# Performance work log

Hardware: AMD Instinct MI355X
Metric: run time of the kernel (lower is better)

The kernel has to match this reference:

```python
import jax, jax.numpy as jnp
import numpy as np

B, T = 256, 20          # batch, sequence length
D = 128                 # encoder feature dim
H = 256                 # LSTM controller hidden / controller_output_size
KS = 256                # memory key/word size
MEM = 20                # memory slots
KNN = 4                 # k-NN addressing
Y = 4                   # output classes (y_dim)
EPS = 1e-8


def setup_inputs() -> dict:
    key = jax.random.key(0)
    ks = jax.random.split(key, 16)
    def kn(k, shape, fan_in):  # kaiming-normal-ish init
        return jax.random.normal(k, shape, jnp.float32) * np.float32(np.sqrt(2.0 / fan_in))
    return {
        "x": jax.random.normal(ks[0], (B, T, 32, 32), jnp.float32),
        # conv encoder
        "conv1_w": kn(ks[1], (32, 1, 4, 4), 1 * 16),  "conv1_b": jnp.zeros(32, jnp.float32),
        "conv2_w": kn(ks[2], (32, 32, 4, 4), 32 * 16), "conv2_b": jnp.zeros(32, jnp.float32),
        "conv3_w": kn(ks[3], (32, 32, 4, 4), 32 * 16), "conv3_b": jnp.zeros(32, jnp.float32),
        "fc1_w": kn(ks[4], (256, 512), 512), "fc1_b": jnp.zeros(256, jnp.float32),
        "fc2_w": kn(ks[5], (128, 256), 256), "fc2_b": jnp.zeros(128, jnp.float32),
        # context norm
        "gamma": jnp.ones(D, jnp.float32), "beta": jnp.zeros(D, jnp.float32),
        # LSTM controller: input = [z_t(128), read(256)] = 384
        "lstm_wi": kn(ks[6], (4 * H, D + KS), D + KS),
        "lstm_wh": kn(ks[7], (4 * H, H), H),
        "lstm_b": jnp.zeros(4 * H, jnp.float32),
        # head projections
        "wk": kn(ks[8], (KS, H), H),   # read key
        "wwk": kn(ks[9], (KS, H), H),  # write key
        "wv": kn(ks[10], (KS, H), H),  # write value
        # output layer on [h, read]
        "wo": kn(ks[11], (Y, H + KS), H + KS), "wo_b": jnp.zeros(Y, jnp.float32),
        "mem_init": jax.random.normal(ks[12], (MEM, KS), jnp.float32) * 0.01,
    }


def _conv(h, w, b):
    out = jax.lax.conv_general_dilated(h, w, (2, 2), [(1, 1), (1, 1)],
                                       dimension_numbers=("NCHW", "OIHW", "NCHW"))
    return jax.nn.relu(out + b[None, :, None, None])


def reference(x, conv1_w, conv1_b, conv2_w, conv2_b, conv3_w, conv3_b,
              fc1_w, fc1_b, fc2_w, fc2_b, gamma, beta,
              lstm_wi, lstm_wh, lstm_b, wk, wwk, wv, wo, wo_b, mem_init):
    b, t = x.shape[0], x.shape[1]
    # --- conv encoder on all B*T frames ---
    h = x.reshape(-1, 1, 32, 32)
    h = _conv(h, conv1_w, conv1_b)          # [BT,32,16,16]
    h = _conv(h, conv2_w, conv2_b)          # [BT,32,8,8]
    h = _conv(h, conv3_w, conv3_b)          # [BT,32,4,4]
    h = h.reshape(h.shape[0], -1)           # [BT,512] (NCHW flatten, matches torch)
    h = jax.nn.relu(h @ fc1_w.T + fc1_b)
    z = jax.nn.relu(h @ fc2_w.T + fc2_b).reshape(b, t, D)
    # --- context norm over time dim (torch var is unbiased) ---
    mu = z.mean(1)
    sigma = jnp.sqrt(z.var(1, ddof=1) + EPS)
    z = (z - mu[:, None, :]) / sigma[:, None, :] * gamma + beta
    # --- NTM-style MANN with k-NN addressing, scan over time ---
    zt = jnp.swapaxes(z, 0, 1)              # [T,B,D]
    M0 = jnp.broadcast_to(mem_init, (b, MEM, KS)) + jnp.zeros((b, MEM, KS), jnp.float32)
    carry0 = (jnp.zeros((b, H), jnp.float32), jnp.zeros((b, H), jnp.float32),
              jnp.zeros((b, KS), jnp.float32), M0)

    def step(carry, z_t):
        h_, c_, r_, M = carry
        inp = jnp.concatenate([z_t, r_], -1)
        gates = inp @ lstm_wi.T + h_ @ lstm_wh.T + lstm_b
        ig, fg, gg, og = jnp.split(gates, 4, -1)  # torch LSTM gate order i,f,g,o
        c_ = jax.nn.sigmoid(fg) * c_ + jax.nn.sigmoid(ig) * jnp.tanh(gg)
        h_ = jax.nn.sigmoid(og) * jnp.tanh(c_)
        Mn = M / (jnp.linalg.norm(M, axis=-1, keepdims=True) + EPS)
        def knn(kq):  # cosine sim -> top-k -> softmax weights
            kqn = kq / (jnp.linalg.norm(kq, axis=-1, keepdims=True) + EPS)
            sims = jnp.einsum('bd,bnd->bn', kqn, Mn)
            tv, ti = jax.lax.top_k(sims, KNN)
            return jax.nn.softmax(tv, -1), ti
        # read head
        wr, ir = knn(h_ @ wk.T)
        rows = jnp.take_along_axis(M, ir[..., None], axis=1)   # [B,KNN,KS] gather
        r_new = jnp.einsum('bk,bkd->bd', wr, rows)
        # write head: weighted scatter-add into top-k slots
        ws, iw = knn(h_ @ wwk.T)
        v = jnp.tanh(h_ @ wv.T)
        bidx = jnp.arange(M.shape[0])[:, None]
        M = M.at[bidx, iw].add(ws[..., None] * v[:, None, :])
        y = jnp.concatenate([h_, r_new], -1) @ wo.T + wo_b
        return (h_, c_, r_new, M), y

    _, ys = jax.lax.scan(step, carry0, zt)   # ys: [T,B,Y]
    y_pred_linear = ys[-1]
    return y_pred_linear, jnp.argmax(y_pred_linear, 1)
```

## Files before the change

### kernel.cpp

```cpp
#include <hip/hip_runtime.h>
#include <hip/hip_bf16.h>

#define EPSF 1e-8f

#define OFF_WIT 0
#define N_WIT   393216
#define OFF_WHT 393216
#define N_WHT   262144
#define OFF_PKT 655360
#define N_PKT   196608
#define OFF_F1T 851968
#define N_F1T   131072
#define OFF_F2T 983040
#define N_F2T   32768
#define OFF_Z   1015808
#define N_Z     655360
#define WS_BASE 1671168
#define OFF_GZ  1671168
#define N_GZ    5242880
#define WS_FULL 6914048

__global__ __launch_bounds__(256) void pack_kernel(
    const float* __restrict__ wi, const float* __restrict__ wh,
    const float* __restrict__ wk, const float* __restrict__ wwk,
    const float* __restrict__ wv,
    const float* __restrict__ f1w, const float* __restrict__ f2w,
    float* __restrict__ ws) {
  int id = blockIdx.x * 256 + threadIdx.x;
  if (id < N_WIT) {
    int j = id & 3, r = (id >> 2) & 1023, k4 = id >> 12;
    ws[OFF_WIT + id] = wi[r * 384 + k4 * 4 + j];
    return;
  }
  id -= N_WIT;
  if (id < N_WHT) {
    int j = id & 3, r = (id >> 2) & 1023, k4 = id >> 12;
    ws[OFF_WHT + id] = wh[r * 256 + k4 * 4 + j];
    return;
  }
  id -= N_WHT;
  if (id < N_PKT) {
    int j = id & 3;
    int q = id >> 2;
    int c = q % 768, k4 = q / 768;
    int m = c >> 8, o = c & 255;
    int col = o * 256 + k4 * 4 + j;
    float v = (m == 0) ? wk[col] : (m == 1) ? wwk[col] : wv[col];
    ws[OFF_PKT + id] = v;
    return;
  }
  id -= N_PKT;
  if (id < N_F1T) {
    int m = id & 3, o = (id >> 2) & 255, k4 = id >> 10;
    ws[OFF_F1T + id] = f1w[o * 512 + k4 * 4 + m];
    return;
  }
  id -= N_F1T;
  if (id < N_F2T) {
    int m = id & 3, o = (id >> 2) & 127, k4 = id >> 9;
    ws[OFF_F2T + id] = f2w[o * 256 + k4 * 4 + m];
  }
}

__global__ __launch_bounds__(256) void enc_kernel(
    const float* __restrict__ x,
    const float* __restrict__ w1, const float* __restrict__ b1,
    const float* __restrict__ w2, const float* __restrict__ b2,
    const float* __restrict__ w3, const float* __restrict__ b3,
    const float* __restrict__ f1b, const float* __restrict__ f2b,
    float* __restrict__ ws) {
  __shared__ __align__(16) float xs[1024];
  __shared__ __align__(16) float c1s[512 * 19];
  __shared__ __align__(16) float c2s[256 * 9];
  __shared__ __align__(16) float c3s[512];
  __shared__ __align__(16) float h1s[256];

  const float4* __restrict__ f1T4 = (const float4*)(ws + OFF_F1T);
  const float4* __restrict__ f2T4 = (const float4*)(ws + OFF_F2T);
  float* __restrict__ z = ws + OFF_Z;

  const int f = blockIdx.x;
  const int tid = threadIdx.x;

  for (int i = tid; i < 1024; i += 256) xs[i] = x[f * 1024 + i];
  __syncthreads();

  {
    int oy = tid >> 4, ox = tid & 15;
    float patch[16];
    #pragma unroll
    for (int ky = 0; ky < 4; ++ky) {
      int iy = oy * 2 - 1 + ky;
      #pragma unroll
      for (int kx = 0; kx < 4; ++kx) {
        int ix = ox * 2 - 1 + kx;
        patch[ky * 4 + kx] =
            ((unsigned)iy <= 31u && (unsigned)ix <= 31u) ? xs[iy * 32 + ix] : 0.f;
      }
    }
    for (int oc = 0; oc < 32; ++oc) {
      float acc = b1[oc];
      #pragma unroll
      for (int k = 0; k < 16; ++k) acc = fmaf(patch[k], w1[oc * 16 + k], acc);
      c1s[(oc * 16 + oy) * 19 + ox] = fmaxf(acc, 0.f);
    }
  }
  __syncthreads();

  {
    int pix = tid & 63;
    int og = __builtin_amdgcn_readfirstlane(tid >> 6);
    int oy = pix >> 3, ox = pix & 7;
    float acc[8];
    #pragma unroll
    for (int j = 0; j < 8; ++j) acc[j] = b2[og * 8 + j];
    for (int ic = 0; ic < 32; ++ic) {
      float patch[16];
      #pragma unroll
      for (int ky = 0; ky < 4; ++ky) {
        int iy = oy * 2 - 1 + ky;
        #pragma unroll
        for (int kx = 0; kx < 4; ++kx) {
          int ix = ox * 2 - 1 + kx;
          patch[ky * 4 + kx] = ((unsigned)iy <= 15u && (unsigned)ix <= 15u)
                                   ? c1s[(ic * 16 + iy) * 19 + ix] : 0.f;
        }
      }
      #pragma unroll
      for (int j = 0; j < 8; ++j) {
        const float* wr = w2 + ((og * 8 + j) * 32 + ic) * 16;
        #pragma unroll
        for (int k = 0; k < 16; ++k) acc[j] = fmaf(patch[k], wr[k], acc[j]);
      }
    }
    #pragma unroll
    for (int j = 0; j < 8; ++j)
      c2s[((og * 8 + j) * 8 + oy) * 9 + ox] = fmaxf(acc[j], 0.f);
  }
  __syncthreads();

  {
    int pix = tid & 15, grp = tid >> 4;
    int oy = pix >> 2, ox = pix & 3;
    float a0 = b3[grp * 2], a1 = b3[grp * 2 + 1];
    for (int ic = 0; ic < 32; ++ic) {
      float patch[16];
      #pragma unroll
      for (int ky = 0; ky < 4; ++ky) {
        int iy = oy * 2 - 1 + ky;
        #pragma unroll
        for (int kx = 0; kx < 4; ++kx) {
          int ix = ox * 2 - 1 + kx;
          patch[ky * 4 + kx] = ((unsigned)iy <= 7u && (unsigned)ix <= 7u)
                                   ? c2s[(ic * 8 + iy) * 9 + ix] : 0.f;
        }
      }
      const float4* wa = (const float4*)(w3 + ((grp * 2 + 0) * 32 + ic) * 16);
      const float4* wb = (const float4*)(w3 + ((grp * 2 + 1) * 32 + ic) * 16);
      #pragma unroll
      for (int q = 0; q < 4; ++q) {
        float4 qa = wa[q], qb = wb[q];
        a0 = fmaf(patch[q * 4 + 0], qa.x, a0);
        a0 = fmaf(patch[q * 4 + 1], qa.y, a0);
        a0 = fmaf(patch[q * 4 + 2], qa.z, a0);
        a0 = fmaf(patch[q * 4 + 3], qa.w, a0);
        a1 = fmaf(patch[q * 4 + 0], qb.x, a1);
        a1 = fmaf(patch[q * 4 + 1], qb.y, a1);
        a1 = fmaf(patch[q * 4 + 2], qb.z, a1);
        a1 = fmaf(patch[q * 4 + 3], qb.w, a1);
      }
    }
    c3s[(grp * 2 + 0) * 16 + pix] = fmaxf(a0, 0.f);
    c3s[(grp * 2 + 1) * 16 + pix] = fmaxf(a1, 0.f);
  }
  __syncthreads();

  {
    float acc = f1b[tid];
    #pragma unroll 8
    for (int k4 = 0; k4 < 128; ++k4) {
      float4 cv = ((const float4*)c3s)[k4];
      float4 w = f1T4[k4 * 256 + tid];
      acc = fmaf(w.x, cv.x, acc);
      acc = fmaf(w.y, cv.y, acc);
      acc = fmaf(w.z, cv.z, acc);
      acc = fmaf(w.w, cv.w, acc);
    }
    h1s[tid] = fmaxf(acc, 0.f);
  }
  __syncthreads();

  if (tid < 128) {
    float acc = f2b[tid];
    #pragma unroll 8
    for (int k4 = 0; k4 < 64; ++k4) {
      float4 hv = ((const float4*)h1s)[k4];
      float4 w = f2T4[k4 * 128 + tid];
      acc = fmaf(w.x, hv.x, acc);
      acc = fmaf(w.y, hv.y, acc);
      acc = fmaf(w.z, hv.z, acc);
      acc = fmaf(w.w, hv.w, acc);
    }
    z[f * 128 + tid] = fmaxf(acc, 0.f);
  }
}

__global__ __launch_bounds__(256) void norm_kernel(
    float* __restrict__ ws,
    const float* __restrict__ gamma, const float* __restrict__ beta) {
  float* z = ws + OFF_Z;
  int g = blockIdx.x * 256 + threadIdx.x;
  int b = g >> 7, d = g & 127;
  float vals[20];
  float mu = 0.f;
  #pragma unroll
  for (int t = 0; t < 20; ++t) {
    float v = z[(b * 20 + t) * 128 + d];
    vals[t] = v;
    mu += v;
  }
  mu *= (1.f / 20.f);
  float var = 0.f;
  #pragma unroll
  for (int t = 0; t < 20; ++t) {
    float dd = vals[t] - mu;
    var = fmaf(dd, dd, var);
  }
  var *= (1.f / 19.f);
  float inv = 1.f / sqrtf(var + EPSF);
  float ga = gamma[d], be = beta[d];
  #pragma unroll
  for (int t = 0; t < 20; ++t)
    z[(b * 20 + t) * 128 + d] = fmaf((vals[t] - mu) * inv, ga, be);
}

__global__ __launch_bounds__(512) void gz_kernel(
    const float* __restrict__ ws, const float* __restrict__ lb,
    float* __restrict__ gz) {
  __shared__ __align__(16) float zs[16][128];
  const float4* wiT4 = (const float4*)(ws + OFF_WIT);
  const float* zz = ws + OFF_Z;
  const int tid = threadIdx.x;
  const int f0 = blockIdx.x * 16;

  for (int i = tid; i < 2048; i += 512) zs[i >> 7][i & 127] = zz[f0 * 128 + i];
  __syncthreads();

  float acc0[16], acc1[16];
  const float b0v = lb[tid], b1v = lb[tid + 512];
  #pragma unroll
  for (int f = 0; f < 16; ++f) { acc0[f] = b0v; acc1[f] = b1v; }

  for (int k4 = 0; k4 < 32; ++k4) {
    float4 w0 = wiT4[k4 * 1024 + tid];
    float4 w1 = wiT4[k4 * 1024 + tid + 512];
    #pragma unroll
    for (int f = 0; f < 16; ++f) {
      float4 zv = *(const float4*)&zs[f][k4 * 4];
      acc0[f] = fmaf(w0.x, zv.x, acc0[f]);
      acc0[f] = fmaf(w0.y, zv.y, acc0[f]);
      acc0[f] = fmaf(w0.z, zv.z, acc0[f]);
      acc0[f] = fmaf(w0.w, zv.w, acc0[f]);
      acc1[f] = fmaf(w1.x, zv.x, acc1[f]);
      acc1[f] = fmaf(w1.y, zv.y, acc1[f]);
      acc1[f] = fmaf(w1.z, zv.z, acc1[f]);
      acc1[f] = fmaf(w1.w, zv.w, acc1[f]);
    }
  }
  #pragma unroll
  for (int f = 0; f < 16; ++f) {
    gz[(f0 + f) * 1024 + tid] = acc0[f];
    gz[(f0 + f) * 1024 + 512 + tid] = acc1[f];
  }
}

__global__ __launch_bounds__(1024, 2) void scan_kernel(
    const float* __restrict__ ws, const float* __restrict__ gz,
    const float* __restrict__ lb, const float* __restrict__ wo,
    const float* __restrict__ wob, const float* __restrict__ mem_init,
    float* __restrict__ out) {
  __shared__ float Msh[2][20 * 257];
  __shared__ __align__(16) float gsh[2][1024];
  __shared__ __align__(16) float inp[2][384];
  __shared__ __align__(16) float hsh[2][256];
  __shared__ float kqsh[2][2][256];
  __shared__ float vsh[2][256];
  __shared__ float sims[2][2][20];
  __shared__ float invq[2][2];
  __shared__ float wsel[2][2][4];
  __shared__ int isel[2][2][4];
  __shared__ float ysh[2][4];

  const int r = threadIdx.x;
  const int b0 = blockIdx.x * 2;
  const int rot = ((blockIdx.x >> 3) & 15) << 2;
  const float4* wiT4 = (const float4*)(ws + OFF_WIT);
  const float4* whT4 = (const float4*)(ws + OFF_WHT);
  const float4* pkT4 = (const float4*)(ws + OFF_PKT);
  const float* zz = ws + OFF_Z;
  const int k4s = gz ? 32 : 0;
  const int wiRange = 96 - k4s;

  #pragma unroll
  for (int bl = 0; bl < 2; ++bl)
    for (int idx = r; idx < 5120; idx += 1024)
      Msh[bl][(idx >> 8) * 257 + (idx & 255)] = mem_init[idx];
  if (r < 512) {
    int bl = r >> 8, u = r & 255;
    hsh[bl][u] = 0.f;
    inp[bl][128 + u] = 0.f;
  }
  float c_reg = 0.f;
  const float bias = lb[r];
  __syncthreads();

  for (int t = 0; t < 20; ++t) {
    if (!gz && r < 256) {
      int bl = r >> 7, d = r & 127;
      inp[bl][d] = zz[((b0 + bl) * 20 + t) * 128 + d];
    }
    __syncthreads();

    float a0, a1;
    if (gz) {
      a0 = gz[(b0 * 20 + t) * 1024 + r];
      a1 = gz[((b0 + 1) * 20 + t) * 1024 + r];
    } else {
      a0 = bias;
      a1 = bias;
    }
    {
      const float4* ip0 = (const float4*)inp[0];
      const float4* ip1 = (const float4*)inp[1];
      #pragma unroll 8
      for (int j = 0; j < 64; ++j) {
        int kk = j + rot;
        if (kk >= 64) kk -= 64;
        int k4 = k4s + kk;
        if (k4s == 0 && j == 0) {  }
        float4 w = wiT4[k4 * 1024 + r];
        float4 z0 = ip0[k4], z1 = ip1[k4];
        a0 = fmaf(w.x, z0.x, a0); a1 = fmaf(w.x, z1.x, a1);
        a0 = fmaf(w.y, z0.y, a0); a1 = fmaf(w.y, z1.y, a1);
        a0 = fmaf(w.z, z0.z, a0); a1 = fmaf(w.z, z1.z, a1);
        a0 = fmaf(w.w, z0.w, a0); a1 = fmaf(w.w, z1.w, a1);
      }
      if (!gz) {
        #pragma unroll 8
        for (int k4 = 0; k4 < 32; ++k4) {
          float4 w = wiT4[k4 * 1024 + r];
          float4 z0 = ip0[k4], z1 = ip1[k4];
          a0 = fmaf(w.x, z0.x, a0); a1 = fmaf(w.x, z1.x, a1);
          a0 = fmaf(w.y, z0.y, a0); a1 = fmaf(w.y, z1.y, a1);
          a0 = fmaf(w.z, z0.z, a0); a1 = fmaf(w.z, z1.z, a1);
          a0 = fmaf(w.w, z0.w, a0); a1 = fmaf(w.w, z1.w, a1);
        }
      }
      const float4* hp0 = (const float4*)hsh[0];
      const float4* hp1 = (const float4*)hsh[1];
      #pragma unroll 8
      for (int j = 0; j < 64; ++j) {
        int k4 = j + rot;
        if (k4 >= 64) k4 -= 64;
        float4 w = whT4[k4 * 1024 + r];
        float4 h0 = hp0[k4], h1 = hp1[k4];
        a0 = fmaf(w.x, h0.x, a0); a1 = fmaf(w.x, h1.x, a1);
        a0 = fmaf(w.y, h0.y, a0); a1 = fmaf(w.y, h1.y, a1);
        a0 = fmaf(w.z, h0.z, a0); a1 = fmaf(w.z, h1.z, a1);
        a0 = fmaf(w.w, h0.w, a0); a1 = fmaf(w.w, h1.w, a1);
      }
    }
    gsh[0][r] = a0;
    gsh[1][r] = a1;
    __syncthreads();

    if (r < 512) {
      int bl = r >> 8, u = r & 255;
      float ig = gsh[bl][u], fg = gsh[bl][256 + u];
      float gg = gsh[bl][512 + u], og = gsh[bl][768 + u];
      c_reg = (1.f / (1.f + expf(-fg))) * c_reg +
              (1.f / (1.f + expf(-ig))) * tanhf(gg);
      hsh[bl][u] = (1.f / (1.f + expf(-og))) * tanhf(c_reg);
    }
    __syncthreads();

    if (r < 768) {
      int m = r >> 8, o = r & 255;
      float s0 = 0.f, s1 = 0.f;
      const float4* hp0 = (const float4*)hsh[0];
      const float4* hp1 = (const float4*)hsh[1];
      #pragma unroll 8
      for (int j = 0; j < 64; ++j) {
        int k4 = j + rot;
        if (k4 >= 64) k4 -= 64;
        float4 w = pkT4[k4 * 768 + r];
        float4 h0 = hp0[k4], h1 = hp1[k4];
        s0 = fmaf(w.x, h0.x, s0); s1 = fmaf(w.x, h1.x, s1);
        s0 = fmaf(w.y, h0.y, s0); s1 = fmaf(w.y, h1.y, s1);
        s0 = fmaf(w.z, h0.z, s0); s1 = fmaf(w.z, h1.z, s1);
        s0 = fmaf(w.w, h0.w, s0); s1 = fmaf(w.w, h1.w, s1);
      }
      if (m < 2) {
        kqsh[0][m][o] = s0;
        kqsh[1][m][o] = s1;
      } else {
        vsh[0][o] = tanhf(s0);
        vsh[1][o] = tanhf(s1);
      }
    }
    __syncthreads();

    if (r < 320) {
      int bl = r >= 160;
      int q = bl ? r - 160 : r;
      int n = q >> 3, l = q & 7;
      const float* Mr = &Msh[bl][n * 257];
      float ss = 0.f, s1 = 0.f, s2 = 0.f;
      for (int i = 0; i < 32; ++i) {
        int k = l + 8 * i;
        float m = Mr[k];
        ss = fmaf(m, m, ss);
        s1 = fmaf(kqsh[bl][0][k], m, s1);
        s2 = fmaf(kqsh[bl][1][k], m, s2);
      }
      ss += __shfl_xor(ss, 1); s1 += __shfl_xor(s1, 1); s2 += __shfl_xor(s2, 1);
      ss += __shfl_xor(ss, 2); s1 += __shfl_xor(s1, 2); s2 += __shfl_xor(s2, 2);
      ss += __shfl_xor(ss, 4); s1 += __shfl_xor(s1, 4); s2 += __shfl_xor(s2, 4);
      if (l == 0) {
        float inv = 1.f / (sqrtf(ss) + EPSF);
        sims[bl][0][n] = s1 * inv;
        sims[bl][1][n] = s2 * inv;
      }
    } else if (r < 324) {
      int bl2 = (r - 320) >> 1, hd = r & 1;
      float qq = 0.f;
      for (int k = 0; k < 256; ++k) {
        float q = kqsh[bl2][hd][k];
        qq = fmaf(q, q, qq);
      }
      invq[bl2][hd] = 1.f / (sqrtf(qq) + EPSF);
    }
    __syncthreads();

    if (r < 4) {
      int bl = r >> 1, hd = r & 1;
      const float* sm = sims[bl][hd];
      float inv = invq[bl][hd];
      unsigned mask = 0;
      float tv[4];
      int ti[4];
      for (int j = 0; j < 4; ++j) {
        float best = -3.4e38f;
        int bx = 0;
        for (int n = 0; n < 20; ++n)
          if (!((mask >> n) & 1u) && sm[n] > best) { best = sm[n]; bx = n; }
        mask |= 1u << bx;
        tv[j] = best * inv;
        ti[j] = bx;
      }
      float e0 = 1.f;
      float e1 = expf(tv[1] - tv[0]);
      float e2 = expf(tv[2] - tv[0]);
      float e3 = expf(tv[3] - tv[0]);
      float s = e0 + e1 + e2 + e3;
      wsel[bl][hd][0] = e0 / s; wsel[bl][hd][1] = e1 / s;
      wsel[bl][hd][2] = e2 / s; wsel[bl][hd][3] = e3 / s;
      isel[bl][hd][0] = ti[0]; isel[bl][hd][1] = ti[1];
      isel[bl][hd][2] = ti[2]; isel[bl][hd][3] = ti[3];
    }
    __syncthreads();

    if (r < 512) {
      int bl = r >> 8, u = r & 255;
      float rvv = 0.f;
      #pragma unroll
      for (int j = 0; j < 4; ++j)
        rvv = fmaf(wsel[bl][0][j], Msh[bl][isel[bl][0][j] * 257 + u], rvv);
      float vv = vsh[bl][u];
      #pragma unroll
      for (int j = 0; j < 4; ++j)
        Msh[bl][isel[bl][1][j] * 257 + u] += wsel[bl][1][j] * vv;
      inp[bl][128 + u] = rvv;
    }
    __syncthreads();
  }

  if (r < 8) {
    int bl = r >> 2, o = r & 3;
    float acc = wob[o];
    const float* wr = wo + o * 512;
    for (int k = 0; k < 256; ++k) acc = fmaf(wr[k], hsh[bl][k], acc);
    for (int k = 0; k < 256; ++k) acc = fmaf(wr[256 + k], inp[bl][128 + k], acc);
    ysh[bl][o] = acc;
    out[(b0 + bl) * 4 + o] = acc;
  }
  __syncthreads();
  if (r < 2) {
    float best = ysh[r][0];
    int bx = 0;
    #pragma unroll
    for (int o = 1; o < 4; ++o)
      if (ysh[r][o] > best) { best = ysh[r][o]; bx = o; }
    out[1024 + b0 + r] = (float)bx;
  }
}

__global__ __launch_bounds__(256) void fused_kernel(
    const float* __restrict__ x,
    const float* __restrict__ w1, const float* __restrict__ b1,
    const float* __restrict__ w2, const float* __restrict__ b2,
    const float* __restrict__ w3, const float* __restrict__ b3,
    const float* __restrict__ f1w, const float* __restrict__ f1b,
    const float* __restrict__ f2w, const float* __restrict__ f2b,
    const float* __restrict__ gamma, const float* __restrict__ beta,
    const float* __restrict__ wi, const float* __restrict__ wh,
    const float* __restrict__ lb, const float* __restrict__ wk,
    const float* __restrict__ wwk, const float* __restrict__ wv,
    const float* __restrict__ wo, const float* __restrict__ wob,
    const float* __restrict__ mem_init, float* __restrict__ out) {
  __shared__ float smem[15104];
  __shared__ float simr[20], simw[20], invq[2], wsel[2][4], ysh[4];
  __shared__ int isel[2][4];
  float* z_all = smem;
  float* pool = smem + 2560;
  float* xs = pool;
  float* c1s = pool + 1024;
  float* c2s = pool + 9216;
  float* c3s = pool + 11264;
  float* h1s = pool + 11776;
  float* w1s = pool + 12032;
  float* Msh = pool;
  float* inp = pool + 5140;
  float* hsh = pool + 5524;
  float* kqr = pool + 5780;
  float* kqw = pool + 6036;
  float* vsh = pool + 6292;
  const int tid = threadIdx.x;
  const int b = blockIdx.x;
  for (int i = tid; i < 512; i += 256) w1s[i] = w1[i];
  for (int f = 0; f < 20; ++f) {
    for (int i = tid; i < 1024; i += 256) xs[i] = x[(b * 20 + f) * 1024 + i];
    __syncthreads();
    for (int i = 0; i < 32; ++i) {
      int idx = i * 256 + tid;
      int oc = idx >> 8, pix = idx & 255, oy = pix >> 4, ox = pix & 15;
      float acc = b1[oc];
      for (int ky = 0; ky < 4; ++ky) {
        int iy = oy * 2 - 1 + ky;
        if ((unsigned)iy > 31u) continue;
        for (int kx = 0; kx < 4; ++kx) {
          int ix = ox * 2 - 1 + kx;
          if ((unsigned)ix > 31u) continue;
          acc = fmaf(xs[iy * 32 + ix], w1s[oc * 16 + ky * 4 + kx], acc);
        }
      }
      c1s[idx] = fmaxf(acc, 0.f);
    }
    __syncthreads();
    {
      int oc = tid >> 3, pg = tid & 7;
      float acc[8];
      float bb = b2[oc];
      for (int i = 0; i < 8; ++i) acc[i] = bb;
      for (int ic = 0; ic < 32; ++ic) {
        const float* in = &c1s[ic * 256];
        const float* wv_ = &w2[(oc * 32 + ic) * 16];
        for (int i = 0; i < 8; ++i) {
          int p = pg + 8 * i;
          int oy = p >> 3, ox = p & 7;
          for (int ky = 0; ky < 4; ++ky) {
            int iy = oy * 2 - 1 + ky;
            if ((unsigned)iy > 15u) continue;
            for (int kx = 0; kx < 4; ++kx) {
              int ix = ox * 2 - 1 + kx;
              if ((unsigned)ix > 15u) continue;
              acc[i] = fmaf(in[iy * 16 + ix], wv_[ky * 4 + kx], acc[i]);
            }
          }
        }
      }
      for (int i = 0; i < 8; ++i) c2s[oc * 64 + pg + 8 * i] = fmaxf(acc[i], 0.f);
    }
    __syncthreads();
    {
      int oc = tid >> 3, pg = tid & 7;
      float bb = b3[oc];
      float acc0 = bb, acc1 = bb;
      int p0 = pg, p1 = pg + 8;
      int oy0 = p0 >> 2, ox0 = p0 & 3, oy1 = p1 >> 2, ox1 = p1 & 3;
      for (int ic = 0; ic < 32; ++ic) {
        const float* in = &c2s[ic * 64];
        const float* wv_ = &w3[(oc * 32 + ic) * 16];
        for (int ky = 0; ky < 4; ++ky) {
          int iy0 = oy0 * 2 - 1 + ky, iy1 = oy1 * 2 - 1 + ky;
          for (int kx = 0; kx < 4; ++kx) {
            float w = wv_[ky * 4 + kx];
            int ix0 = ox0 * 2 - 1 + kx, ix1 = ox1 * 2 - 1 + kx;
            if ((unsigned)iy0 <= 7u && (unsigned)ix0 <= 7u)
              acc0 = fmaf(in[iy0 * 8 + ix0], w, acc0);
            if ((unsigned)iy1 <= 7u && (unsigned)ix1 <= 7u)
              acc1 = fmaf(in[iy1 * 8 + ix1], w, acc1);
          }
        }
      }
      c3s[oc * 16 + p0] = fmaxf(acc0, 0.f);
      c3s[oc * 16 + p1] = fmaxf(acc1, 0.f);
    }
    __syncthreads();
    {
      float acc = f1b[tid];
      const float* wr = f1w + tid * 512;
      for (int k = 0; k < 512; ++k) acc = fmaf(wr[k], c3s[k], acc);
      h1s[tid] = fmaxf(acc, 0.f);
    }
    __syncthreads();
    if (tid < 128) {
      float acc = f2b[tid];
      const float* wr = f2w + tid * 256;
      for (int k = 0; k < 256; ++k) acc = fmaf(wr[k], h1s[k], acc);
      z_all[f * 128 + tid] = fmaxf(acc, 0.f);
    }
    __syncthreads();
  }
  if (tid < 128) {
    float mu = 0.f;
    for (int t = 0; t < 20; ++t) mu += z_all[t * 128 + tid];
    mu *= (1.f / 20.f);
    float var = 0.f;
    for (int t = 0; t < 20; ++t) {
      float dd = z_all[t * 128 + tid] - mu;
      var = fmaf(dd, dd, var);
    }
    var *= (1.f / 19.f);
    float inv = 1.f / sqrtf(var + EPSF);
    float ga = gamma[tid], be = beta[tid];
    for (int t = 0; t < 20; ++t)
      z_all[t * 128 + tid] = fmaf((z_all[t * 128 + tid] - mu) * inv, ga, be);
  }
  for (int idx = tid; idx < 20 * 256; idx += 256)
    Msh[(idx >> 8) * 257 + (idx & 255)] = mem_init[idx];
  hsh[tid] = 0.f;
  inp[128 + tid] = 0.f;
  float c_reg = 0.f;
  __syncthreads();
  const int u = tid;
  for (int t = 0; t < 20; ++t) {
    if (u < 128) inp[u] = z_all[t * 128 + u];
    __syncthreads();
    float a[4];
    for (int g = 0; g < 4; ++g) {
      int row = g * 256 + u;
      float acc = lb[row];
      const float* wr = wi + row * 384;
      for (int k = 0; k < 384; ++k) acc = fmaf(wr[k], inp[k], acc);
      const float* hr = wh + row * 256;
      for (int k = 0; k < 256; ++k) acc = fmaf(hr[k], hsh[k], acc);
      a[g] = acc;
    }
    __syncthreads();
    {
      float ig = 1.f / (1.f + expf(-a[0]));
      float fg = 1.f / (1.f + expf(-a[1]));
      float gg = tanhf(a[2]);
      float og = 1.f / (1.f + expf(-a[3]));
      c_reg = fg * c_reg + ig * gg;
      hsh[u] = og * tanhf(c_reg);
    }
    __syncthreads();
    {
      float sk = 0.f, sw = 0.f, sv = 0.f;
      const float* rk = wk + u * 256;
      const float* rw = wwk + u * 256;
      const float* rv = wv + u * 256;
      for (int k = 0; k < 256; ++k) {
        float hv = hsh[k];
        sk = fmaf(rk[k], hv, sk);
        sw = fmaf(rw[k], hv, sw);
        sv = fmaf(rv[k], hv, sv);
      }
      kqr[u] = sk;
      kqw[u] = sw;
      vsh[u] = tanhf(sv);
    }
    __syncthreads();
    if (u < 20) {
      const float* Mr = &Msh[u * 257];
      float ss = 0.f, s1 = 0.f, s2 = 0.f;
      for (int k = 0; k < 256; ++k) {
        float m = Mr[k];
        ss = fmaf(m, m, ss);
        s1 = fmaf(kqr[k], m, s1);
        s2 = fmaf(kqw[k], m, s2);
      }
      float inv = 1.f / (sqrtf(ss) + EPSF);
      simr[u] = s1 * inv;
      simw[u] = s2 * inv;
    } else if (u == 20 || u == 21) {
      const float* q = (u == 20) ? kqr : kqw;
      float qq = 0.f;
      for (int k = 0; k < 256; ++k) qq = fmaf(q[k], q[k], qq);
      invq[u - 20] = 1.f / (sqrtf(qq) + EPSF);
    }
    __syncthreads();
    if (u < 2) {
      const float* sims = (u == 0) ? simr : simw;
      float inv = invq[u];
      unsigned mask = 0;
      float tv[4];
      int ti[4];
      for (int j = 0; j < 4; ++j) {
        float best = -3.4e38f;
        int bx = 0;
        for (int n = 0; n < 20; ++n)
          if (!((mask >> n) & 1u) && sims[n] > best) { best = sims[n]; bx = n; }
        mask |= 1u << bx;
        tv[j] = best * inv;
        ti[j] = bx;
      }
      float e1 = expf(tv[1] - tv[0]);
      float e2 = expf(tv[2] - tv[0]);
      float e3 = expf(tv[3] - tv[0]);
      float s = 1.f + e1 + e2 + e3;
      wsel[u][0] = 1.f / s; wsel[u][1] = e1 / s; wsel[u][2] = e2 / s; wsel[u][3] = e3 / s;
      isel[u][0] = ti[0]; isel[u][1] = ti[1]; isel[u][2] = ti[2]; isel[u][3] = ti[3];
    }
    __syncthreads();
    {
      float rvv = 0.f;
      for (int j = 0; j < 4; ++j)
        rvv = fmaf(wsel[0][j], Msh[isel[0][j] * 257 + u], rvv);
      float vv = vsh[u];
      for (int j = 0; j < 4; ++j)
        Msh[isel[1][j] * 257 + u] += wsel[1][j] * vv;
      inp[128 + u] = rvv;
    }
    __syncthreads();
  }
  if (u < 4) {
    float acc = wob[u];
    const float* wr = wo + u * 512;
    for (int k = 0; k < 256; ++k) acc = fmaf(wr[k], hsh[k], acc);
    for (int k = 0; k < 256; ++k) acc = fmaf(wr[256 + k], inp[128 + k], acc);
    ysh[u] = acc;
    out[b * 4 + u] = acc;
  }
  __syncthreads();
  if (u == 0) {
    float best = ysh[0];
    int bx = 0;
    for (int o = 1; o < 4; ++o)
      if (ysh[o] > best) { best = ysh[o]; bx = o; }
    out[1024 + b] = (float)bx;
  }
}

extern "C" void kernel_launch(void* const* d_in, const int* in_sizes, int n_in,
                              void* d_out, int out_size, void* d_ws, size_t ws_size,
                              hipStream_t stream) {
  const float* x    = (const float*)d_in[0];
  const float* c1w  = (const float*)d_in[1];
  const float* c1b  = (const float*)d_in[2];
  const float* c2w  = (const float*)d_in[3];
  const float* c2b  = (const float*)d_in[4];
  const float* c3w  = (const float*)d_in[5];
  const float* c3b  = (const float*)d_in[6];
  const float* f1w  = (const float*)d_in[7];
  const float* f1b  = (const float*)d_in[8];
  const float* f2w  = (const float*)d_in[9];
  const float* f2b  = (const float*)d_in[10];
  const float* gam  = (const float*)d_in[11];
  const float* bet  = (const float*)d_in[12];
  const float* wi   = (const float*)d_in[13];
  const float* wh   = (const float*)d_in[14];
  const float* lb   = (const float*)d_in[15];
  const float* wk   = (const float*)d_in[16];
  const float* wwk  = (const float*)d_in[17];
  const float* wv   = (const float*)d_in[18];
  const float* wo   = (const float*)d_in[19];
  const float* wob  = (const float*)d_in[20];
  const float* mem0 = (const float*)d_in[21];
  float* out = (float*)d_out;

  if (ws_size >= (size_t)WS_BASE * sizeof(float)) {
    float* ws = (float*)d_ws;
    const bool full = ws_size >= (size_t)WS_FULL * sizeof(float);
    pack_kernel<<<3968, 256, 0, stream>>>(wi, wh, wk, wwk, wv, f1w, f2w, ws);
    enc_kernel<<<5120, 256, 0, stream>>>(x, c1w, c1b, c2w, c2b, c3w, c3b,
                                         f1b, f2b, ws);
    norm_kernel<<<128, 256, 0, stream>>>(ws, gam, bet);
    const float* gz = nullptr;
    if (full) {
      gz_kernel<<<320, 512, 0, stream>>>(ws, lb, ws + OFF_GZ);
      gz = ws + OFF_GZ;
    }
    scan_kernel<<<128, 1024, 0, stream>>>(ws, gz, lb, wo, wob, mem0, out);
  } else {
    fused_kernel<<<256, 256, 0, stream>>>(x, c1w, c1b, c2w, c2b, c3w, c3b,
                                          f1w, f1b, f2w, f2b, gam, bet,
                                          wi, wh, lb, wk, wwk, wv, wo, wob,
                                          mem0, out);
  }
}
```

Before: 1.277 ms.

## Batch four frames per encoder block for FC weight reuse; nontemporal scan weight loads

The encoder kernel now runs the conv stack for four frames in sequence inside each block and keeps their conv3 and fc1 outputs in shared memory. The fc1 and fc2 layers then load each weight float4 once and apply it to all four frames, cutting global weight traffic for those layers by four. The grid shrinks from 5120 to 1280 blocks, which lowers parallelism for the conv part. Separately, the scan kernel's LSTM and projection weight loads use nontemporal load builtins, which changes their cache behaviour.

```diff
diff --git a/kernel.cpp b/kernel.cpp
--- a/kernel.cpp
+++ b/kernel.cpp
@@ -2,6 +2,8 @@
 #include <hip/hip_bf16.h>
 
 #define EPSF 1e-8f
+
+typedef float nt4 __attribute__((ext_vector_type(4)));
 
 #define OFF_WIT 0
 #define N_WIT   393216
@@ -72,49 +74,22 @@
   __shared__ __align__(16) float xs[1024];
   __shared__ __align__(16) float c1s[512 * 19];
   __shared__ __align__(16) float c2s[256 * 9];
-  __shared__ __align__(16) float c3s[512];
-  __shared__ __align__(16) float h1s[256];
+  __shared__ __align__(16) float c3s[4][512];
+  __shared__ __align__(16) float h1s[4][256];
 
   const float4* __restrict__ f1T4 = (const float4*)(ws + OFF_F1T);
   const float4* __restrict__ f2T4 = (const float4*)(ws + OFF_F2T);
   float* __restrict__ z = ws + OFF_Z;
 
-  const int f = blockIdx.x;
   const int tid = threadIdx.x;
 
-  for (int i = tid; i < 1024; i += 256) xs[i] = x[f * 1024 + i];
-  __syncthreads();
-
-  {
-    int oy = tid >> 4, ox = tid & 15;
-    float patch[16];
-    #pragma unroll
-    for (int ky = 0; ky < 4; ++ky) {
-      int iy = oy * 2 - 1 + ky;
-      #pragma unroll
-      for (int kx = 0; kx < 4; ++kx) {
-        int ix = ox * 2 - 1 + kx;
-        patch[ky * 4 + kx] =
-            ((unsigned)iy <= 31u && (unsigned)ix <= 31u) ? xs[iy * 32 + ix] : 0.f;
-      }
-    }
-    for (int oc = 0; oc < 32; ++oc) {
-      float acc = b1[oc];
-      #pragma unroll
-      for (int k = 0; k < 16; ++k) acc = fmaf(patch[k], w1[oc * 16 + k], acc);
-      c1s[(oc * 16 + oy) * 19 + ox] = fmaxf(acc, 0.f);
-    }
-  }
-  __syncthreads();
-
-  {
-    int pix = tid & 63;
-    int og = __builtin_amdgcn_readfirstlane(tid >> 6);
-    int oy = pix >> 3, ox = pix & 7;
-    float acc[8];
-    #pragma unroll
-    for (int j = 0; j < 8; ++j) acc[j] = b2[og * 8 + j];
-    for (int ic = 0; ic < 32; ++ic) {
+  for (int ff = 0; ff < 4; ++ff) {
+    const int f = blockIdx.x * 4 + ff;
+    for (int i = tid; i < 1024; i += 256) xs[i] = x[f * 1024 + i];
+    __syncthreads();
+
+    {
+      int oy = tid >> 4, ox = tid & 15;
       float patch[16];
       #pragma unroll
       for (int ky = 0; ky < 4; ++ky) {
@@ -122,86 +97,130 @@
         #pragma unroll
         for (int kx = 0; kx < 4; ++kx) {
           int ix = ox * 2 - 1 + kx;
-          patch[ky * 4 + kx] = ((unsigned)iy <= 15u && (unsigned)ix <= 15u)
-                                   ? c1s[(ic * 16 + iy) * 19 + ix] : 0.f;
+          patch[ky * 4 + kx] =
+              ((unsigned)iy <= 31u && (unsigned)ix <= 31u) ? xs[iy * 32 + ix] : 0.f;
         }
       }
+      for (int oc = 0; oc < 32; ++oc) {
+        float acc = b1[oc];
+        #pragma unroll
+        for (int k = 0; k < 16; ++k) acc = fmaf(patch[k], w1[oc * 16 + k], acc);
+        c1s[(oc * 16 + oy) * 19 + ox] = fmaxf(acc, 0.f);
+      }
+    }
+    __syncthreads();
+
+    {
+      int pix = tid & 63;
+      int og = __builtin_amdgcn_readfirstlane(tid >> 6);
+      int oy = pix >> 3, ox = pix & 7;
+      float acc[8];
       #pragma unroll
-      for (int j = 0; j < 8; ++j) {
-        const float* wr = w2 + ((og * 8 + j) * 32 + ic) * 16;
+      for (int j = 0; j < 8; ++j) acc[j] = b2[og * 8 + j];
+      for (int ic = 0; ic < 32; ++ic) {
+        float patch[16];
         #pragma unroll
-        for (int k = 0; k < 16; ++k) acc[j] = fmaf(patch[k], wr[k], acc[j]);
-      }
-    }
+        for (int ky = 0; ky < 4; ++ky) {
+          int iy = oy * 2 - 1 + ky;
+          #pragma unroll
+          for (int kx = 0; kx < 4; ++kx) {
+            int ix = ox * 2 - 1 + kx;
+            patch[ky * 4 + kx] = ((unsigned)iy <= 15u && (unsigned)ix <= 15u)
+                                     ? c1s[(ic * 16 + iy) * 19 + ix] : 0.f;
+          }
+        }
+        #pragma unroll
+        for (int j = 0; j < 8; ++j) {
+          const float* wr = w2 + ((og * 8 + j) * 32 + ic) * 16;
+          #pragma unroll
+          for (int k = 0; k < 16; ++k) acc[j] = fmaf(patch[k], wr[k], acc[j]);
+        }
+      }
+      #pragma unroll
+      for (int j = 0; j < 8; ++j)
+        c2s[((og * 8 + j) * 8 + oy) * 9 + ox] = fmaxf(acc[j], 0.f);
+    }
+    __syncthreads();
+
+    {
+      int pix = tid & 15, grp = tid >> 4;
+      int oy = pix >> 2, ox = pix & 3;
+      float a0 = b3[grp * 2], a1 = b3[grp * 2 + 1];
+      for (int ic = 0; ic < 32; ++ic) {
+        float patch[16];
+        #pragma unroll
+        for (int ky = 0; ky < 4; ++ky) {
+          int iy = oy * 2 - 1 + ky;
+          #pragma unroll
+          for (int kx = 0; kx < 4; ++kx) {
+            int ix = ox * 2 - 1 + kx;
+            patch[ky * 4 + kx] = ((unsigned)iy <= 7u && (unsigned)ix <= 7u)
+                                     ? c2s[(ic * 8 + iy) * 9 + ix] : 0.f;
+          }
+        }
+        const float4* wa = (const float4*)(w3 + ((grp * 2 + 0) * 32 + ic) * 16);
+        const float4* wb = (const float4*)(w3 + ((grp * 2 + 1) * 32 + ic) * 16);
+        #pragma unroll
+        for (int q = 0; q < 4; ++q) {
+          float4 qa = wa[q], qb = wb[q];
+          a0 = fmaf(patch[q * 4 + 0], qa.x, a0);
+          a0 = fmaf(patch[q * 4 + 1], qa.y, a0);
+          a0 = fmaf(patch[q * 4 + 2], qa.z, a0);
+          a0 = fmaf(patch[q * 4 + 3], qa.w, a0);
+          a1 = fmaf(patch[q * 4 + 0], qb.x, a1);
+          a1 = fmaf(patch[q * 4 + 1], qb.y, a1);
+          a1 = fmaf(patch[q * 4 + 2], qb.z, a1);
+          a1 = fmaf(patch[q * 4 + 3], qb.w, a1);
+        }
+      }
+      c3s[ff][(grp * 2 + 0) * 16 + pix] = fmaxf(a0, 0.f);
+      c3s[ff][(grp * 2 + 1) * 16 + pix] = fmaxf(a1, 0.f);
+    }
+    __syncthreads();
+  }
+
+  {
+    float acc[4];
+    float bb = f1b[tid];
     #pragma unroll
-    for (int j = 0; j < 8; ++j)
-      c2s[((og * 8 + j) * 8 + oy) * 9 + ox] = fmaxf(acc[j], 0.f);
+    for (int ff = 0; ff < 4; ++ff) acc[ff] = bb;
+    #pragma unroll 4
+    for (int k4 = 0; k4 < 128; ++k4) {
+      float4 w = f1T4[k4 * 256 + tid];
+      #pragma unroll
+      for (int ff = 0; ff < 4; ++ff) {
+        float4 cv = ((const float4*)c3s[ff])[k4];
+        acc[ff] = fmaf(w.x, cv.x, acc[ff]);
+        acc[ff] = fmaf(w.y, cv.y, acc[ff]);
+        acc[ff] = fmaf(w.z, cv.z, acc[ff]);
+        acc[ff] = fmaf(w.w, cv.w, acc[ff]);
+      }
+    }
+    #pragma unroll
+    for (int ff = 0; ff < 4; ++ff) h1s[ff][tid] = fmaxf(acc[ff], 0.f);
   }
   __syncthreads();
 
-  {
-    int pix = tid & 15, grp = tid >> 4;
-    int oy = pix >> 2, ox = pix & 3;
-    float a0 = b3[grp * 2], a1 = b3[grp * 2 + 1];
-    for (int ic = 0; ic < 32; ++ic) {
-      float patch[16];
+  if (tid < 128) {
+    float acc[4];
+    float bb = f2b[tid];
+    #pragma unroll
+    for (int ff = 0; ff < 4; ++ff) acc[ff] = bb;
+    #pragma unroll 4
+    for (int k4 = 0; k4 < 64; ++k4) {
+      float4 w = f2T4[k4 * 128 + tid];
       #pragma unroll
-      for (int ky = 0; ky < 4; ++ky) {
-        int iy = oy * 2 - 1 + ky;
-        #pragma unroll
-        for (int kx = 0; kx < 4; ++kx) {
-          int ix = ox * 2 - 1 + kx;
-          patch[ky * 4 + kx] = ((unsigned)iy <= 7u && (unsigned)ix <= 7u)
-                                   ? c2s[(ic * 8 + iy) * 9 + ix] : 0.f;
-        }
-      }
-      const float4* wa = (const float4*)(w3 + ((grp * 2 + 0) * 32 + ic) * 16);
-      const float4* wb = (const float4*)(w3 + ((grp * 2 + 1) * 32 + ic) * 16);
-      #pragma unroll
-      for (int q = 0; q < 4; ++q) {
-        float4 qa = wa[q], qb = wb[q];
-        a0 = fmaf(patch[q * 4 + 0], qa.x, a0);
-        a0 = fmaf(patch[q * 4 + 1], qa.y, a0);
-        a0 = fmaf(patch[q * 4 + 2], qa.z, a0);
-        a0 = fmaf(patch[q * 4 + 3], qa.w, a0);
-        a1 = fmaf(patch[q * 4 + 0], qb.x, a1);
-        a1 = fmaf(patch[q * 4 + 1], qb.y, a1);
-        a1 = fmaf(patch[q * 4 + 2], qb.z, a1);
-        a1 = fmaf(patch[q * 4 + 3], qb.w, a1);
-      }
-    }
-    c3s[(grp * 2 + 0) * 16 + pix] = fmaxf(a0, 0.f);
-    c3s[(grp * 2 + 1) * 16 + pix] = fmaxf(a1, 0.f);
-  }
-  __syncthreads();
-
-  {
-    float acc = f1b[tid];
-    #pragma unroll 8
-    for (int k4 = 0; k4 < 128; ++k4) {
-      float4 cv = ((const float4*)c3s)[k4];
-      float4 w = f1T4[k4 * 256 + tid];
-      acc = fmaf(w.x, cv.x, acc);
-      acc = fmaf(w.y, cv.y, acc);
-      acc = fmaf(w.z, cv.z, acc);
-      acc = fmaf(w.w, cv.w, acc);
-    }
-    h1s[tid] = fmaxf(acc, 0.f);
-  }
-  __syncthreads();
-
-  if (tid < 128) {
-    float acc = f2b[tid];
-    #pragma unroll 8
-    for (int k4 = 0; k4 < 64; ++k4) {
-      float4 hv = ((const float4*)h1s)[k4];
-      float4 w = f2T4[k4 * 128 + tid];
-      acc = fmaf(w.x, hv.x, acc);
-      acc = fmaf(w.y, hv.y, acc);
-      acc = fmaf(w.z, hv.z, acc);
-      acc = fmaf(w.w, hv.w, acc);
-    }
-    z[f * 128 + tid] = fmaxf(acc, 0.f);
+      for (int ff = 0; ff < 4; ++ff) {
+        float4 hv = ((const float4*)h1s[ff])[k4];
+        acc[ff] = fmaf(w.x, hv.x, acc[ff]);
+        acc[ff] = fmaf(w.y, hv.y, acc[ff]);
+        acc[ff] = fmaf(w.z, hv.z, acc[ff]);
+        acc[ff] = fmaf(w.w, hv.w, acc[ff]);
+      }
+    }
+    #pragma unroll
+    for (int ff = 0; ff < 4; ++ff)
+      z[(blockIdx.x * 4 + ff) * 128 + tid] = fmaxf(acc[ff], 0.f);
   }
 }
 
@@ -294,12 +313,11 @@
   const int r = threadIdx.x;
   const int b0 = blockIdx.x * 2;
   const int rot = ((blockIdx.x >> 3) & 15) << 2;
-  const float4* wiT4 = (const float4*)(ws + OFF_WIT);
-  const float4* whT4 = (const float4*)(ws + OFF_WHT);
-  const float4* pkT4 = (const float4*)(ws + OFF_PKT);
+  const nt4* wiT4 = (const nt4*)(ws + OFF_WIT);
+  const nt4* whT4 = (const nt4*)(ws + OFF_WHT);
+  const nt4* pkT4 = (const nt4*)(ws + OFF_PKT);
   const float* zz = ws + OFF_Z;
   const int k4s = gz ? 32 : 0;
-  const int wiRange = 96 - k4s;
 
   #pragma unroll
   for (int bl = 0; bl < 2; ++bl)
@@ -337,8 +355,7 @@
         int kk = j + rot;
         if (kk >= 64) kk -= 64;
         int k4 = k4s + kk;
-        if (k4s == 0 && j == 0) {  }
-        float4 w = wiT4[k4 * 1024 + r];
+        nt4 w = __builtin_nontemporal_load(&wiT4[k4 * 1024 + r]);
         float4 z0 = ip0[k4], z1 = ip1[k4];
         a0 = fmaf(w.x, z0.x, a0); a1 = fmaf(w.x, z1.x, a1);
         a0 = fmaf(w.y, z0.y, a0); a1 = fmaf(w.y, z1.y, a1);
@@ -348,7 +365,7 @@
       if (!gz) {
         #pragma unroll 8
         for (int k4 = 0; k4 < 32; ++k4) {
-          float4 w = wiT4[k4 * 1024 + r];
+          nt4 w = __builtin_nontemporal_load(&wiT4[k4 * 1024 + r]);
           float4 z0 = ip0[k4], z1 = ip1[k4];
           a0 = fmaf(w.x, z0.x, a0); a1 = fmaf(w.x, z1.x, a1);
           a0 = fmaf(w.y, z0.y, a0); a1 = fmaf(w.y, z1.y, a1);
@@ -362,7 +379,7 @@
       for (int j = 0; j < 64; ++j) {
         int k4 = j + rot;
         if (k4 >= 64) k4 -= 64;
-        float4 w = whT4[k4 * 1024 + r];
+        nt4 w = __builtin_nontemporal_load(&whT4[k4 * 1024 + r]);
         float4 h0 = hp0[k4], h1 = hp1[k4];
         a0 = fmaf(w.x, h0.x, a0); a1 = fmaf(w.x, h1.x, a1);
         a0 = fmaf(w.y, h0.y, a0); a1 = fmaf(w.y, h1.y, a1);
@@ -393,7 +410,7 @@
       for (int j = 0; j < 64; ++j) {
         int k4 = j + rot;
         if (k4 >= 64) k4 -= 64;
-        float4 w = pkT4[k4 * 768 + r];
+        nt4 w = __builtin_nontemporal_load(&pkT4[k4 * 768 + r]);
         float4 h0 = hp0[k4], h1 = hp1[k4];
         s0 = fmaf(w.x, h0.x, s0); s1 = fmaf(w.x, h1.x, s1);
         s0 = fmaf(w.y, h0.y, s0); s1 = fmaf(w.y, h1.y, s1);
@@ -785,7 +802,7 @@
     float* ws = (float*)d_ws;
     const bool full = ws_size >= (size_t)WS_FULL * sizeof(float);
     pack_kernel<<<3968, 256, 0, stream>>>(wi, wh, wk, wwk, wv, f1w, f2w, ws);
-    enc_kernel<<<5120, 256, 0, stream>>>(x, c1w, c1b, c2w, c2b, c3w, c3b,
+    enc_kernel<<<1280, 256, 0, stream>>>(x, c1w, c1b, c2w, c2b, c3w, c3b,
                                          f1b, f2b, ws);
     norm_kernel<<<128, 256, 0, stream>>>(ws, gam, bet);
     const float* gz = nullptr;
```

Result: slower. 1.920 ms (+50.3%).
